# Performance work log

Hardware: AMD Instinct MI355X
Metric: run time of the kernel (lower is better)

Reference implementation:

```python
import jax, jax.numpy as jnp
import numpy as np

GROUP_SIZE = 32
FP8_MAX = 448.0
EPS = 1e-8


def fp8_pseudo_quantize_groupwise(x):
    """Per-group (contiguous groups of GROUP_SIZE along last dim) fp8-e4m3
    pseudo-quantization: scale to fp8 range, cast to fp8, cast back, rescale."""
    shape = x.shape
    g = shape[-1] // GROUP_SIZE
    xg = x.reshape(*shape[:-1], g, GROUP_SIZE)
    amax = jnp.max(jnp.abs(xg), axis=-1, keepdims=True)
    scale = jnp.maximum(amax, EPS) / FP8_MAX  # fp32 per-group scale
    q = (xg / scale).astype(jnp.float8_e4m3fn).astype(x.dtype)
    return (q * scale).reshape(shape)


def setup_inputs() -> dict:
    key = jax.random.key(0)
    k1, k2, k3 = jax.random.split(key, 3)
    B, S, K, N = 4, 2048, 4096, 4096
    x = jax.random.normal(k1, (B, S, K), dtype=jnp.float32)
    # Linear-like init scale for weight/bias
    W = jax.random.normal(k2, (N, K), dtype=jnp.float32) * (1.0 / np.sqrt(K))
    bias = jax.random.normal(k3, (N,), dtype=jnp.float32) * (1.0 / np.sqrt(K))
    return {"x": x, "W": W, "bias": bias}


def reference(x, W, bias):
    # pseudo mode, a_bit=8 < 16: quantize both activations and weight
    Wq = fp8_pseudo_quantize_groupwise(W)   # [N, K]
    xq = fp8_pseudo_quantize_groupwise(x)   # [B, S, K]
    # F.linear: xq @ Wq.T + bias
    out = jnp.einsum('bsk,nk->bsn', xq, Wq) + bias
    return out
```

## Files before the change

kernel.cpp:

```cpp
#include <hip/hip_runtime.h>
#include <hip/hip_bf16.h>

typedef __bf16 bf16x8 __attribute__((ext_vector_type(8)));
typedef float floatx4 __attribute__((ext_vector_type(4)));
typedef unsigned short ushortx8 __attribute__((ext_vector_type(8)));

#define FP8_MAX 448.0f
#define QEPS 1e-8f

#define GLLDS16(gptr, lptr)                                                          \
  __builtin_amdgcn_global_load_lds((const __attribute__((address_space(1))) void*)(gptr), \
                                   (__attribute__((address_space(3))) void*)(lptr), 16, 0, 0)

__global__ __launch_bounds__(256) void quant_dq_kernel(
    const float* __restrict__ src, __hip_bfloat16* __restrict__ dst, long long n)
{
    long long t = (long long)blockIdx.x * blockDim.x + threadIdx.x;
    long long base = t * 8;
    if (base >= n) return;

    const float4 v0 = *(const float4*)(src + base);
    const float4 v1 = *(const float4*)(src + base + 4);

    float am = fmaxf(
        fmaxf(fmaxf(fabsf(v0.x), fabsf(v0.y)), fmaxf(fabsf(v0.z), fabsf(v0.w))),
        fmaxf(fmaxf(fabsf(v1.x), fabsf(v1.y)), fmaxf(fabsf(v1.z), fabsf(v1.w))));
    am = fmaxf(am, __shfl_xor(am, 1));
    am = fmaxf(am, __shfl_xor(am, 2));
    const float scale = fmaxf(am, QEPS) / FP8_MAX;

    int p0 = __builtin_amdgcn_cvt_pk_fp8_f32(v0.x / scale, v0.y / scale, 0, false);
    int p1 = __builtin_amdgcn_cvt_pk_fp8_f32(v0.z / scale, v0.w / scale, 0, false);
    int p2 = __builtin_amdgcn_cvt_pk_fp8_f32(v1.x / scale, v1.y / scale, 0, false);
    int p3 = __builtin_amdgcn_cvt_pk_fp8_f32(v1.z / scale, v1.w / scale, 0, false);

    float r0 = __builtin_amdgcn_cvt_f32_fp8(p0, 0) * scale;
    float r1 = __builtin_amdgcn_cvt_f32_fp8(p0, 1) * scale;
    float r2 = __builtin_amdgcn_cvt_f32_fp8(p1, 0) * scale;
    float r3 = __builtin_amdgcn_cvt_f32_fp8(p1, 1) * scale;
    float r4 = __builtin_amdgcn_cvt_f32_fp8(p2, 0) * scale;
    float r5 = __builtin_amdgcn_cvt_f32_fp8(p2, 1) * scale;
    float r6 = __builtin_amdgcn_cvt_f32_fp8(p3, 0) * scale;
    float r7 = __builtin_amdgcn_cvt_f32_fp8(p3, 1) * scale;

    alignas(16) __hip_bfloat16 hb[8] = {
        __float2bfloat16(r0), __float2bfloat16(r1),
        __float2bfloat16(r2), __float2bfloat16(r3),
        __float2bfloat16(r4), __float2bfloat16(r5),
        __float2bfloat16(r6), __float2bfloat16(r7)};
    *(ushortx8*)(dst + base) = *(const ushortx8*)hb;
}


#define BAR() __builtin_amdgcn_s_barrier()
#define VMCNT(n) asm volatile("s_waitcnt vmcnt(" #n ")" ::: "memory")

#define STAGE_A(a_, t_, b_)                                                   \
  do {                                                                        \
    const __hip_bfloat16* g_ = gAs + (long)(a_) * 128 * K + (long)(t_) * 64;  \
    __hip_bfloat16* l_ = &sA[(b_)][(a_) * 8192 + tid * 8];                    \
    GLLDS16(g_, l_);                                                          \
    GLLDS16(g_ + 64 * (long)K, l_ + 4096);                                    \
  } while (0)

#define STAGE_B(a_, t_, b_)                                                   \
  do {                                                                        \
    const __hip_bfloat16* g_ = gBs + (long)(a_) * 128 * K + (long)(t_) * 64;  \
    __hip_bfloat16* l_ = &sB[(b_)][(a_) * 8192 + tid * 8];                    \
    GLLDS16(g_, l_);                                                          \
    GLLDS16(g_ + 64 * (long)K, l_ + 4096);                                    \
  } while (0)

#define STAGE_TILE(t_, b_)                                                    \
  do {                                                                        \
    STAGE_A(0, t_, b_); STAGE_A(1, t_, b_);                                   \
    STAGE_B(0, t_, b_); STAGE_B(1, t_, b_);                                   \
  } while (0)

#define LOAD_A(buf, mh)                                                       \
  do {                                                                        \
    _Pragma("unroll") for (int mm = 0; mm < 4; ++mm)                          \
    _Pragma("unroll") for (int ks = 0; ks < 2; ++ks)                          \
        af[mm][ks] = *(const bf16x8*)((buf) + ((mh)*4 + mm) * 1024 + aoff[ks]); \
  } while (0)

#define LOAD_B(buf, nh)                                                       \
  do {                                                                        \
    _Pragma("unroll") for (int nn = 0; nn < 2; ++nn)                          \
    _Pragma("unroll") for (int ks = 0; ks < 2; ++ks)                          \
        bfr[nh][nn][ks] = *(const bf16x8*)((buf) + (nh)*2048 + nn * 1024 + boff[ks]); \
  } while (0)

#define QUAD(mh, nh)                                                          \
  do {                                                                        \
    __builtin_amdgcn_s_setprio(1);                                            \
    _Pragma("unroll") for (int ks = 0; ks < 2; ++ks)                          \
    _Pragma("unroll") for (int mm = 0; mm < 4; ++mm)                          \
    _Pragma("unroll") for (int nn = 0; nn < 2; ++nn)                          \
        acc[(mh)*4 + mm][(nh)*2 + nn] = __builtin_amdgcn_mfma_f32_16x16x32_bf16( \
            af[mm][ks], bfr[nh][nn][ks], acc[(mh)*4 + mm][(nh)*2 + nn], 0, 0, 0); \
    __builtin_amdgcn_s_setprio(0);                                            \
  } while (0)

#define COMPUTE(bufA, bufB)                                                   \
  do {                                                                        \
    LOAD_A(bufA, 0); LOAD_B(bufB, 0);                                         \
    QUAD(0, 0);                                                               \
    LOAD_B(bufB, 1);                                                          \
    QUAD(0, 1);                                                               \
    LOAD_A(bufA, 1);                                                          \
    QUAD(1, 0);                                                               \
    QUAD(1, 1);                                                               \
  } while (0)

__global__ __launch_bounds__(512, 2) void gemm_bias_kernel(
    const __hip_bfloat16* __restrict__ A,
    const __hip_bfloat16* __restrict__ B,
    const float* __restrict__ bias,
    float* __restrict__ C,
    int M, int N, int K)
{
    __shared__ __attribute__((aligned(16))) __hip_bfloat16 sA[2][256 * 64];
    __shared__ __attribute__((aligned(16))) __hip_bfloat16 sB[2][256 * 64];

    const int tid  = threadIdx.x;
    const int lane = tid & 63;
    const int wave = tid >> 6;
    const int wm   = wave >> 2;
    const int wn   = wave & 3;

    const int nwg = gridDim.x;
    const int wg  = blockIdx.x;
    int swz = wg;
    if ((nwg & 7) == 0) swz = (wg & 7) * (nwg >> 3) + (wg >> 3);
    const int NXB = N >> 8;
    const long bm = (long)(swz / NXB) * 256;
    const long bn = (long)(swz % NXB) * 256;

    const int srow   = tid >> 3;
    const int schunk = (tid & 7) ^ (srow & 7);
    const __hip_bfloat16* gAs = A + (bm + srow) * (long)K + schunk * 8;
    const __hip_bfloat16* gBs = B + (bn + srow) * (long)K + schunk * 8;

    const int fr = lane & 15;
    const int fq = lane >> 4;
    const int f7 = fr & 7;
    int aoff[2], boff[2];
#pragma unroll
    for (int ks = 0; ks < 2; ++ks) {
        const int ch = ((ks * 4 + fq) ^ f7) * 8;
        aoff[ks] = (wm * 128 + fr) * 64 + ch;
        boff[ks] = (wn * 64 + fr) * 64 + ch;
    }

    floatx4 acc[8][4];
#pragma unroll
    for (int i = 0; i < 8; ++i)
#pragma unroll
        for (int j = 0; j < 4; ++j)
            acc[i][j] = (floatx4){0.f, 0.f, 0.f, 0.f};

    bf16x8 af[4][2];
    bf16x8 bfr[2][2][2];

    const int NT = K >> 6;
    const int NI = NT >> 1;

    STAGE_TILE(0, 0);
    VMCNT(0);
    BAR();

#pragma unroll 1
    for (int i = 0; i < NI; ++i) {
        STAGE_TILE(2 * i + 1, 1);
        COMPUTE(sA[0], sB[0]);
        VMCNT(0);
        BAR();

        if (i + 1 < NI) STAGE_TILE(2 * i + 2, 0);
        COMPUTE(sA[1], sB[1]);
        VMCNT(0);
        BAR();
    }

    const int rq = (lane >> 4) * 4;
#pragma unroll
    for (int j = 0; j < 4; ++j) {
        const long gc = bn + wn * 64 + j * 16 + fr;
        const float bj = bias[gc];
#pragma unroll
        for (int mf = 0; mf < 8; ++mf) {
            const long gr = bm + wm * 128 + mf * 16 + rq;
            float* cp = C + gr * (long)N + gc;
#pragma unroll
            for (int r = 0; r < 4; ++r)
                cp[(long)r * N] = acc[mf][j][r] + bj;
        }
    }
}

extern "C" void kernel_launch(void* const* d_in, const int* in_sizes, int n_in,
                              void* d_out, int out_size, void* d_ws, size_t ws_size,
                              hipStream_t stream) {
    const float* x    = (const float*)d_in[0];
    const float* W    = (const float*)d_in[1];
    const float* bias = (const float*)d_in[2];
    float* out = (float*)d_out;

    const long long nx = in_sizes[0];
    const long long nw = in_sizes[1];
    const int N = in_sizes[2];
    const int K = (int)(nw / N);
    const int M = (int)(nx / K);

    __hip_bfloat16* xq = (__hip_bfloat16*)d_ws;
    __hip_bfloat16* wq = xq + nx;

    {
        long long tx = nx / 8;
        int blocks = (int)((tx + 255) / 256);
        quant_dq_kernel<<<blocks, 256, 0, stream>>>(x, xq, nx);
    }
    {
        long long tw = nw / 8;
        int blocks = (int)((tw + 255) / 256);
        quant_dq_kernel<<<blocks, 256, 0, stream>>>(W, wq, nw);
    }

    dim3 grid((N / 256) * (M / 256));
    gemm_bias_kernel<<<grid, 512, 0, stream>>>(xq, wq, bias, out, M, N, K);
}
```

Before: 536.1 us.

## Shrink GEMM block tile to 256x128 with K-step 32 and 4 waves

The GEMM block tile changes from 256x256 with 8 waves and a K-step of 64 to 256x128 with 4 waves and a K-step of 32. Each wave still computes a 128x64 output, but it loads all fragments at once and issues a single 8x4 MFMA block per stage. The shared-memory swizzle is redone for the narrower 32-element rows. LDS use drops to about a quarter, which may allow more resident blocks. The cost is twice as many barrier/stage iterations and more redundant global reads of A and B, since each block covers fewer output columns.

```diff
diff --git a/kernel.cpp b/kernel.cpp
--- a/kernel.cpp
+++ b/kernel.cpp
@@ -55,103 +55,65 @@
 #define BAR() __builtin_amdgcn_s_barrier()
 #define VMCNT(n) asm volatile("s_waitcnt vmcnt(" #n ")" ::: "memory")
 
-#define STAGE_A(a_, t_, b_)                                                   \
+#define STAGE_TILE(t_, b_)                                                    \
   do {                                                                        \
-    const __hip_bfloat16* g_ = gAs + (long)(a_) * 128 * K + (long)(t_) * 64;  \
-    __hip_bfloat16* l_ = &sA[(b_)][(a_) * 8192 + tid * 8];                    \
-    GLLDS16(g_, l_);                                                          \
-    GLLDS16(g_ + 64 * (long)K, l_ + 4096);                                    \
+    _Pragma("unroll") for (int r_ = 0; r_ < 4; ++r_)                          \
+        GLLDS16(gAs + (long)r_ * 64 * K + (long)(t_) * 32,                    \
+                &sA[(b_)][r_ * 2048 + tid * 8]);                              \
+    _Pragma("unroll") for (int r_ = 0; r_ < 2; ++r_)                          \
+        GLLDS16(gBs + (long)r_ * 64 * K + (long)(t_) * 32,                    \
+                &sB[(b_)][r_ * 2048 + tid * 8]);                              \
   } while (0)
 
-#define STAGE_B(a_, t_, b_)                                                   \
+#define COMPUTE(b_)                                                           \
   do {                                                                        \
-    const __hip_bfloat16* g_ = gBs + (long)(a_) * 128 * K + (long)(t_) * 64;  \
-    __hip_bfloat16* l_ = &sB[(b_)][(a_) * 8192 + tid * 8];                    \
-    GLLDS16(g_, l_);                                                          \
-    GLLDS16(g_ + 64 * (long)K, l_ + 4096);                                    \
-  } while (0)
-
-#define STAGE_TILE(t_, b_)                                                    \
-  do {                                                                        \
-    STAGE_A(0, t_, b_); STAGE_A(1, t_, b_);                                   \
-    STAGE_B(0, t_, b_); STAGE_B(1, t_, b_);                                   \
-  } while (0)
-
-#define LOAD_A(buf, mh)                                                       \
-  do {                                                                        \
-    _Pragma("unroll") for (int mm = 0; mm < 4; ++mm)                          \
-    _Pragma("unroll") for (int ks = 0; ks < 2; ++ks)                          \
-        af[mm][ks] = *(const bf16x8*)((buf) + ((mh)*4 + mm) * 1024 + aoff[ks]); \
-  } while (0)
-
-#define LOAD_B(buf, nh)                                                       \
-  do {                                                                        \
-    _Pragma("unroll") for (int nn = 0; nn < 2; ++nn)                          \
-    _Pragma("unroll") for (int ks = 0; ks < 2; ++ks)                          \
-        bfr[nh][nn][ks] = *(const bf16x8*)((buf) + (nh)*2048 + nn * 1024 + boff[ks]); \
-  } while (0)
-
-#define QUAD(mh, nh)                                                          \
-  do {                                                                        \
+    bf16x8 af[8], bfv[4];                                                     \
+    _Pragma("unroll") for (int i_ = 0; i_ < 8; ++i_)                          \
+        af[i_] = *(const bf16x8*)(&sA[(b_)][aoff0 + i_ * 512]);               \
+    _Pragma("unroll") for (int j_ = 0; j_ < 4; ++j_)                          \
+        bfv[j_] = *(const bf16x8*)(&sB[(b_)][boff0 + j_ * 512]);              \
     __builtin_amdgcn_s_setprio(1);                                            \
-    _Pragma("unroll") for (int ks = 0; ks < 2; ++ks)                          \
-    _Pragma("unroll") for (int mm = 0; mm < 4; ++mm)                          \
-    _Pragma("unroll") for (int nn = 0; nn < 2; ++nn)                          \
-        acc[(mh)*4 + mm][(nh)*2 + nn] = __builtin_amdgcn_mfma_f32_16x16x32_bf16( \
-            af[mm][ks], bfr[nh][nn][ks], acc[(mh)*4 + mm][(nh)*2 + nn], 0, 0, 0); \
+    _Pragma("unroll") for (int i_ = 0; i_ < 8; ++i_)                          \
+    _Pragma("unroll") for (int j_ = 0; j_ < 4; ++j_)                          \
+        acc[i_][j_] = __builtin_amdgcn_mfma_f32_16x16x32_bf16(                \
+            af[i_], bfv[j_], acc[i_][j_], 0, 0, 0);                           \
     __builtin_amdgcn_s_setprio(0);                                            \
   } while (0)
 
-#define COMPUTE(bufA, bufB)                                                   \
-  do {                                                                        \
-    LOAD_A(bufA, 0); LOAD_B(bufB, 0);                                         \
-    QUAD(0, 0);                                                               \
-    LOAD_B(bufB, 1);                                                          \
-    QUAD(0, 1);                                                               \
-    LOAD_A(bufA, 1);                                                          \
-    QUAD(1, 0);                                                               \
-    QUAD(1, 1);                                                               \
-  } while (0)
-
-__global__ __launch_bounds__(512, 2) void gemm_bias_kernel(
+__global__ __launch_bounds__(256, 2) void gemm_bias_kernel(
     const __hip_bfloat16* __restrict__ A,
     const __hip_bfloat16* __restrict__ B,
     const float* __restrict__ bias,
     float* __restrict__ C,
     int M, int N, int K)
 {
-    __shared__ __attribute__((aligned(16))) __hip_bfloat16 sA[2][256 * 64];
-    __shared__ __attribute__((aligned(16))) __hip_bfloat16 sB[2][256 * 64];
+    __shared__ __attribute__((aligned(16))) __hip_bfloat16 sA[2][256 * 32];
+    __shared__ __attribute__((aligned(16))) __hip_bfloat16 sB[2][128 * 32];
 
     const int tid  = threadIdx.x;
     const int lane = tid & 63;
     const int wave = tid >> 6;
-    const int wm   = wave >> 2;
-    const int wn   = wave & 3;
+    const int wm   = wave >> 1;
+    const int wn   = wave & 1;
 
     const int nwg = gridDim.x;
     const int wg  = blockIdx.x;
     int swz = wg;
     if ((nwg & 7) == 0) swz = (wg & 7) * (nwg >> 3) + (wg >> 3);
-    const int NXB = N >> 8;
+    const int NXB = N >> 7;
     const long bm = (long)(swz / NXB) * 256;
-    const long bn = (long)(swz % NXB) * 256;
+    const long bn = (long)(swz % NXB) * 128;
 
-    const int srow   = tid >> 3;
-    const int schunk = (tid & 7) ^ (srow & 7);
+    const int srow   = tid >> 2;
+    const int schunk = (tid & 3) ^ ((srow >> 1) & 3);
     const __hip_bfloat16* gAs = A + (bm + srow) * (long)K + schunk * 8;
     const __hip_bfloat16* gBs = B + (bn + srow) * (long)K + schunk * 8;
 
     const int fr = lane & 15;
     const int fq = lane >> 4;
-    const int f7 = fr & 7;
-    int aoff[2], boff[2];
-#pragma unroll
-    for (int ks = 0; ks < 2; ++ks) {
-        const int ch = ((ks * 4 + fq) ^ f7) * 8;
-        aoff[ks] = (wm * 128 + fr) * 64 + ch;
-        boff[ks] = (wn * 64 + fr) * 64 + ch;
-    }
+    const int ach  = (fq ^ ((fr >> 1) & 3)) * 8;
+    const int aoff0 = (wm * 128 + fr) * 32 + ach;
+    const int boff0 = (wn * 64 + fr) * 32 + ach;
 
     floatx4 acc[8][4];
 #pragma unroll
@@ -160,11 +122,7 @@
         for (int j = 0; j < 4; ++j)
             acc[i][j] = (floatx4){0.f, 0.f, 0.f, 0.f};
 
-    bf16x8 af[4][2];
-    bf16x8 bfr[2][2][2];
-
-    const int NT = K >> 6;
-    const int NI = NT >> 1;
+    const int NI = K >> 6;
 
     STAGE_TILE(0, 0);
     VMCNT(0);
@@ -173,12 +131,12 @@
 #pragma unroll 1
     for (int i = 0; i < NI; ++i) {
         STAGE_TILE(2 * i + 1, 1);
-        COMPUTE(sA[0], sB[0]);
+        COMPUTE(0);
         VMCNT(0);
         BAR();
 
         if (i + 1 < NI) STAGE_TILE(2 * i + 2, 0);
-        COMPUTE(sA[1], sB[1]);
+        COMPUTE(1);
         VMCNT(0);
         BAR();
     }
@@ -227,6 +185,6 @@
         quant_dq_kernel<<<blocks, 256, 0, stream>>>(W, wq, nw);
     }
 
-    dim3 grid((N / 256) * (M / 256));
-    gemm_bias_kernel<<<grid, 512, 0, stream>>>(xq, wq, bias, out, M, N, K);
+    dim3 grid((N / 128) * (M / 256));
+    gemm_bias_kernel<<<grid, 256, 0, stream>>>(xq, wq, bias, out, M, N, K);
 }
```

Result: slower. 578.3 us (+7.9%).
